# Performance work log

Measured on AMD Instinct MI355X. Metric: run time of the kernel, lower is better.

The kernel has to match this reference:

```python
import jax, jax.numpy as jnp
import numpy as np

EPS = 0.1
MAX_ITER = 100
THRESH = 0.1


def setup_inputs() -> dict:
    key = jax.random.key(0)
    k1, k2, k3, k4 = jax.random.split(key, 4)
    N, P1, P2, D = 4, 1024, 1024, 16
    x = jax.random.normal(k1, (N, P1, D), dtype=jnp.float32)
    y = jax.random.normal(k2, (N, P2, D), dtype=jnp.float32)
    wx = jax.random.uniform(k3, (N, P1), dtype=jnp.float32)
    wy = jax.random.uniform(k4, (N, P2), dtype=jnp.float32)
    # normalize to probability weights (typical usage for empirical measures)
    wx = wx / jnp.sum(wx, axis=-1, keepdims=True)
    wy = wy / jnp.sum(wy, axis=-1, keepdims=True)
    return {"x": x, "y": y, "wx": wx, "wy": wy}


def _cost_matrix(x, y):
    # |x_i - y_j|^1 summed over feature dim -> [N, P1, P2]
    return jnp.sum(jnp.abs(x[:, :, None, :] - y[:, None, :, :]), axis=-1)


def reference(x, y, wx, wy):
    C = _cost_matrix(x, y)                     # [N, P1, P2]
    mu, nu = wx, wy                            # [N, P1], [N, P2]
    log_mu = jnp.log(mu + 1e-8)
    log_nu = jnp.log(nu + 1e-8)

    def M(u, v):
        # (-C_ij + u_i + v_j) / eps
        return (-C + u[:, :, None] + v[:, None, :]) / EPS

    def step(carry, _):
        u, v, done = carry
        u_new = EPS * (log_mu - jax.nn.logsumexp(M(u, v), axis=-1)) + u
        v_new = EPS * (log_nu - jax.nn.logsumexp(M(u_new, v), axis=-2)) + v
        err = jnp.mean(jnp.sum(jnp.abs(u_new - u), axis=-1))
        # emulate torch's early break: freeze u,v once converged
        u_out = jnp.where(done, u, u_new)
        v_out = jnp.where(done, v, v_new)
        done = done | (err < THRESH)
        return (u_out, v_out, done), None

    u0 = jnp.zeros_like(mu)
    v0 = jnp.zeros_like(nu)
    (u, v, _), _ = jax.lax.scan(step, (u0, v0, jnp.array(False)), None, length=MAX_ITER)

    pi = jnp.exp(M(u, v))                      # transport plan [N, P1, P2]
    cost = jnp.sum(pi * C, axis=(-2, -1))      # [N]  (reduction='none')
    return cost, pi, C
```

## Files before the change

### kernel.cpp

```cpp
#include <hip/hip_runtime.h>

static constexpr int   NB      = 4;
static constexpr int   PP      = 1024;
static constexpr int   DD      = 16;
static constexpr float EPSV    = 0.1f;
static constexpr float KE      = 14.42695041f;
static constexpr float KL      = 0.0693147181f;
static constexpr int   MAXIT   = 100;
static constexpr float THRESHV = 0.1f;

static constexpr int NBLK = 256;
static constexpr int NTHR = 512;
static constexpr unsigned DONEG = 1000000u;

__device__ __forceinline__ float fexp2(float v) { return __builtin_amdgcn_exp2f(v); }
__device__ __forceinline__ float flog2(float v) { return __builtin_amdgcn_logf(v); }

static constexpr int    ERR_F_OFF     = 4352;
static constexpr size_t WS_ZERO_BYTES = 4352 * 4;
static constexpr size_t ERR_BYTES    = 512 * 4;

static constexpr int VSNAP_OFF = 131072;

__device__ __forceinline__ float aload(const float* p) {
    return __hip_atomic_load(p, __ATOMIC_RELAXED, __HIP_MEMORY_SCOPE_AGENT);
}
__device__ __forceinline__ void astore(float* p, float v) {
    __hip_atomic_store(p, v, __ATOMIC_RELAXED, __HIP_MEMORY_SCOPE_AGENT);
}
__device__ __forceinline__ unsigned aloadu(const unsigned* p) {
    return __hip_atomic_load(p, __ATOMIC_RELAXED, __HIP_MEMORY_SCOPE_AGENT);
}
__device__ __forceinline__ void astoreu(unsigned* p, unsigned v) {
    __hip_atomic_store(p, v, __ATOMIC_RELAXED, __HIP_MEMORY_SCOPE_AGENT);
}
__device__ __forceinline__ float2 aload2(const float* p) {
    unsigned long long v = __hip_atomic_load((const unsigned long long*)p,
                                             __ATOMIC_RELAXED, __HIP_MEMORY_SCOPE_AGENT);
    union { unsigned long long u; float f[2]; } c; c.u = v;
    return make_float2(c.f[0], c.f[1]);
}
__device__ __forceinline__ void astore2(float* p, float a, float b) {
    union { unsigned long long u; float f[2]; } c; c.f[0] = a; c.f[1] = b;
    __hip_atomic_store((unsigned long long*)p, c.u,
                       __ATOMIC_RELAXED, __HIP_MEMORY_SCOPE_AGENT);
}

__device__ __forceinline__ void gbar_group(unsigned* ws32, int n, int g, unsigned gen) {
    __syncthreads();
    if (threadIdx.x < 64) {
        if (threadIdx.x == 0) astoreu(ws32 + (n * 64 + g) * 16, gen);
        const unsigned* sp = ws32 + (n * 64 + threadIdx.x) * 16;
        while (__ballot(aloadu(sp) >= gen) != ~0ull)
            __builtin_amdgcn_s_sleep(1);
    }
    __syncthreads();
}

__global__ __launch_bounds__(NTHR, 2)
void sinkhorn_kernel(const float* __restrict__ x, const float* __restrict__ y,
                     const float* __restrict__ wx, const float* __restrict__ wy,
                     float* __restrict__ out, float* __restrict__ ws)
{
    __shared__ float rt[16 * PP];
    __shared__ float sbuf[PP];
    __shared__ float cred[8];
    __shared__ int   Ts;

    unsigned* ws32  = (unsigned*)ws;
    unsigned* Tslot = ws32 + 4096;
    unsigned* exitf = ws32 + 4104;
    float*    ews   = ws + ERR_F_OFF;

    float* out_cost = out;
    float* out_pi   = out + NB;
    float* out_C    = out + NB + (size_t)NB * PP * PP;

    const int b   = blockIdx.x;
    const int n   = b >> 6;
    const int g   = b & 63;
    const int i0  = g * 16;
    const int w   = threadIdx.x >> 6;
    const int l   = threadIdx.x & 63;
    const int tid = threadIdx.x;

    float* sc = out_C + (size_t)n * PP * PP;

    float4 xr[2][4];
    #pragma unroll
    for (int rr = 0; rr < 2; ++rr) {
        const float4* xp = (const float4*)(x + ((size_t)n * PP + (i0 + 2 * w + rr)) * DD);
        #pragma unroll
        for (int q = 0; q < 4; ++q) xr[rr][q] = xp[q];
    }
    #pragma unroll 4
    for (int k = 0; k < 16; ++k) {
        int j = l + 64 * k;
        const float4* yp = (const float4*)(y + ((size_t)n * PP + j) * DD);
        float4 y0 = yp[0], y1 = yp[1], y2 = yp[2], y3 = yp[3];
        #pragma unroll
        for (int rr = 0; rr < 2; ++rr) {
            float c = fabsf(xr[rr][0].x - y0.x) + fabsf(xr[rr][0].y - y0.y)
                    + fabsf(xr[rr][0].z - y0.z) + fabsf(xr[rr][0].w - y0.w)
                    + fabsf(xr[rr][1].x - y1.x) + fabsf(xr[rr][1].y - y1.y)
                    + fabsf(xr[rr][1].z - y1.z) + fabsf(xr[rr][1].w - y1.w)
                    + fabsf(xr[rr][2].x - y2.x) + fabsf(xr[rr][2].y - y2.y)
                    + fabsf(xr[rr][2].z - y2.z) + fabsf(xr[rr][2].w - y2.w)
                    + fabsf(xr[rr][3].x - y3.x) + fabsf(xr[rr][3].y - y3.y)
                    + fabsf(xr[rr][3].z - y3.z) + fabsf(xr[rr][3].w - y3.w);
            rt[(2 * w + rr) * PP + j] = c;
        }
    }

    float4 yc[2][4];
    #pragma unroll
    for (int c = 0; c < 2; ++c) {
        const float4* yp = (const float4*)(y + ((size_t)n * PP + (i0 + 2 * w + c)) * DD);
        #pragma unroll
        for (int q = 0; q < 4; ++q) yc[c][q] = yp[q];
    }
    float2 c2[16];
    #pragma unroll 4
    for (int k = 0; k < 16; ++k) {
        const float4* xp = (const float4*)(x + ((size_t)n * PP + (l + 64 * k)) * DD);
        float4 x0 = xp[0], x1 = xp[1], x2 = xp[2], x3 = xp[3];
        float cc[2];
        #pragma unroll
        for (int c = 0; c < 2; ++c) {
            cc[c] = fabsf(x0.x - yc[c][0].x) + fabsf(x0.y - yc[c][0].y)
                  + fabsf(x0.z - yc[c][0].z) + fabsf(x0.w - yc[c][0].w)
                  + fabsf(x1.x - yc[c][1].x) + fabsf(x1.y - yc[c][1].y)
                  + fabsf(x1.z - yc[c][1].z) + fabsf(x1.w - yc[c][1].w)
                  + fabsf(x2.x - yc[c][2].x) + fabsf(x2.y - yc[c][2].y)
                  + fabsf(x2.z - yc[c][2].z) + fabsf(x2.w - yc[c][2].w)
                  + fabsf(x3.x - yc[c][3].x) + fabsf(x3.y - yc[c][3].y)
                  + fabsf(x3.z - yc[c][3].z) + fabsf(x3.w - yc[c][3].w);
        }
        c2[k] = make_float2(cc[0], cc[1]);
    }

    float lmu[2], lnu[2];
    #pragma unroll
    for (int rr = 0; rr < 2; ++rr) {
        lmu[rr] = __logf(wx[n * PP + i0 + 2 * w + rr] + 1e-8f);
        lnu[rr] = __logf(wy[n * PP + i0 + 2 * w + rr] + 1e-8f);
    }

    float uprev0 = 0.f, uprev1 = 0.f;

    #pragma unroll 1
    for (int t = 0; t < MAXIT; ++t) {
        if (t >= 2) {
            unsigned ef = aloadu(exitf + n);
            if (ef != 0u && t >= (int)ef + 1) break;
        }

        if (t == 0) {
            sbuf[2 * tid] = 0.f; sbuf[2 * tid + 1] = 0.f;
        } else {
            float2 vp = aload2(sc + VSNAP_OFF + (size_t)(t - 1) * PP + 2 * tid);
            sbuf[2 * tid] = vp.x; sbuf[2 * tid + 1] = vp.y;
        }
        __syncthreads();

        {
            float4 tt[2][4];
            float m0 = -3.4e38f, m1 = -3.4e38f;
            #pragma unroll
            for (int k = 0; k < 4; ++k) {
                int j = 256 * k + 4 * l;
                float4 v4 = *(const float4*)&sbuf[j];
                float4 ca = *(const float4*)&rt[(2 * w) * PP + j];
                float4 cb = *(const float4*)&rt[(2 * w + 1) * PP + j];
                tt[0][k] = make_float4(v4.x - ca.x, v4.y - ca.y, v4.z - ca.z, v4.w - ca.w);
                tt[1][k] = make_float4(v4.x - cb.x, v4.y - cb.y, v4.z - cb.z, v4.w - cb.w);
                m0 = fmaxf(m0, fmaxf(fmaxf(tt[0][k].x, tt[0][k].y), fmaxf(tt[0][k].z, tt[0][k].w)));
                m1 = fmaxf(m1, fmaxf(fmaxf(tt[1][k].x, tt[1][k].y), fmaxf(tt[1][k].z, tt[1][k].w)));
            }
            #pragma unroll
            for (int off = 32; off >= 1; off >>= 1) {
                m0 = fmaxf(m0, __shfl_xor(m0, off));
                m1 = fmaxf(m1, __shfl_xor(m1, off));
            }
            float s0 = 0.f, s1 = 0.f;
            #pragma unroll
            for (int k = 0; k < 4; ++k) {
                s0 += fexp2((tt[0][k].x - m0) * KE) + fexp2((tt[0][k].y - m0) * KE)
                    + fexp2((tt[0][k].z - m0) * KE) + fexp2((tt[0][k].w - m0) * KE);
                s1 += fexp2((tt[1][k].x - m1) * KE) + fexp2((tt[1][k].y - m1) * KE)
                    + fexp2((tt[1][k].z - m1) * KE) + fexp2((tt[1][k].w - m1) * KE);
            }
            #pragma unroll
            for (int off = 32; off >= 1; off >>= 1) {
                s0 += __shfl_xor(s0, off);
                s1 += __shfl_xor(s1, off);
            }
            float un0 = EPSV * lmu[0] - (m0 + KL * flog2(s0));
            float un1 = EPSV * lmu[1] - (m1 + KL * flog2(s1));
            if (l == 0) astore2(sc + (size_t)t * PP + i0 + 2 * w, un0, un1);
        }

        gbar_group(ws32, n, g, (unsigned)(2 * t + 1));

        {
            float2 up = aload2(sc + (size_t)t * PP + 2 * tid);
            sbuf[2 * tid] = up.x; sbuf[2 * tid + 1] = up.y;
            float we = fabsf(up.x - uprev0) + fabsf(up.y - uprev1);
            uprev0 = up.x; uprev1 = up.y;
            #pragma unroll
            for (int off = 32; off >= 1; off >>= 1) we += __shfl_xor(we, off);
            if (l == 0) cred[w] = we;
        }
        __syncthreads();

        {
            float tt0[16], tt1[16], m0 = -3.4e38f, m1 = -3.4e38f;
            #pragma unroll
            for (int k = 0; k < 16; ++k) {
                float uu = sbuf[l + 64 * k];
                tt0[k] = uu - c2[k].x;
                tt1[k] = uu - c2[k].y;
                m0 = fmaxf(m0, tt0[k]);
                m1 = fmaxf(m1, tt1[k]);
            }
            #pragma unroll
            for (int off = 32; off >= 1; off >>= 1) {
                m0 = fmaxf(m0, __shfl_xor(m0, off));
                m1 = fmaxf(m1, __shfl_xor(m1, off));
            }
            float s0 = 0.f, s1 = 0.f;
            #pragma unroll
            for (int k = 0; k < 16; ++k) {
                s0 += fexp2((tt0[k] - m0) * KE);
                s1 += fexp2((tt1[k] - m1) * KE);
            }
            #pragma unroll
            for (int off = 32; off >= 1; off >>= 1) {
                s0 += __shfl_xor(s0, off);
                s1 += __shfl_xor(s1, off);
            }
            float vn0 = EPSV * lnu[0] - (m0 + KL * flog2(s0));
            float vn1 = EPSV * lnu[1] - (m1 + KL * flog2(s1));
            if (l == 0)
                astore2(sc + VSNAP_OFF + (size_t)t * PP + i0 + 2 * w, vn0, vn1);
        }
        if (g == 0 && tid == 0) {
            float es = cred[0] + cred[1] + cred[2] + cred[3]
                     + cred[4] + cred[5] + cred[6] + cred[7];
            astore(ews + n * 128 + t, es);
        }

        __syncthreads();
        if (tid < 64) {
            if (tid == 0) astoreu(ws32 + (n * 64 + g) * 16, (unsigned)(2 * t + 2));
            if (g == 0) {
                float s1f = aload(ews + 0 * 128 + tid) + aload(ews + 1 * 128 + tid)
                          + aload(ews + 2 * 128 + tid) + aload(ews + 3 * 128 + tid);
                float s2f = aload(ews + 0 * 128 + 64 + tid) + aload(ews + 1 * 128 + 64 + tid)
                          + aload(ews + 2 * 128 + 64 + tid) + aload(ews + 3 * 128 + 64 + tid);
                unsigned long long bb = __ballot(s1f < THRESHV * (float)NB)
                                      | __ballot(s2f < THRESHV * (float)NB);
                if (bb != 0ull && tid == 0 && aloadu(exitf + n) == 0u)
                    astoreu(exitf + n, (unsigned)(t + 1));
            }
            const unsigned* sp = ws32 + (n * 64 + tid) * 16;
            while (__ballot(aloadu(sp) >= (unsigned)(2 * t + 2)) != ~0ull)
                __builtin_amdgcn_s_sleep(1);
        }
        __syncthreads();
    }

    if (g == 0 && tid == 0) astoreu(ws32 + (n * 64) * 16, DONEG);

    if (b == 0 && tid < 64) {
        for (;;) {
            bool ok = (tid >= 4) || (aloadu(ws32 + tid * 64 * 16) >= DONEG);
            if (__ballot(ok) == ~0ull) break;
            __builtin_amdgcn_s_sleep(2);
        }
        float s1f = aload(ews + 0 * 128 + tid) + aload(ews + 1 * 128 + tid)
                  + aload(ews + 2 * 128 + tid) + aload(ews + 3 * 128 + tid);
        float s2f = aload(ews + 0 * 128 + 64 + tid) + aload(ews + 1 * 128 + 64 + tid)
                  + aload(ews + 2 * 128 + 64 + tid) + aload(ews + 3 * 128 + 64 + tid);
        unsigned long long b1 = __ballot(s1f < THRESHV * (float)NB);
        unsigned long long b2 = __ballot(s2f < THRESHV * (float)NB);
        int T = b1 ? (__ffsll((long long)b1) - 1)
                   : (b2 ? 64 + (__ffsll((long long)b2) - 1) : MAXIT - 1);
        if (tid == 0) astoreu(Tslot, (unsigned)(T + 1));
    }
    if (tid == 0) {
        unsigned tv;
        while ((tv = aloadu(Tslot)) == 0u) __builtin_amdgcn_s_sleep(2);
        Ts = (int)tv - 1;
    }
    __syncthreads();
    const int T = Ts;

    float u_loc[2];
    {
        float2 up = aload2(sc + (size_t)T * PP + i0 + 2 * w);
        u_loc[0] = up.x; u_loc[1] = up.y;
        float2 vp = aload2(sc + VSNAP_OFF + (size_t)T * PP + 2 * tid);
        sbuf[2 * tid] = vp.x; sbuf[2 * tid + 1] = vp.y;
    }
    gbar_group(ws32, n, g, DONEG + 1u);

    float cacc = 0.f;
    #pragma unroll
    for (int rr = 0; rr < 2; ++rr) {
        int r = 2 * w + rr;
        int i = i0 + r;
        float un = u_loc[rr];
        #pragma unroll
        for (int k = 0; k < 4; ++k) {
            int j = 256 * k + 4 * l;
            float4 c4 = *(const float4*)&rt[r * PP + j];
            float4 v4 = *(const float4*)&sbuf[j];
            float4 p4;
            p4.x = fexp2((un + v4.x - c4.x) * KE);
            p4.y = fexp2((un + v4.y - c4.y) * KE);
            p4.z = fexp2((un + v4.z - c4.z) * KE);
            p4.w = fexp2((un + v4.w - c4.w) * KE);
            *(float4*)&out_pi[((size_t)n * PP + i) * PP + j] = p4;
            *(float4*)&out_C [((size_t)n * PP + i) * PP + j] = c4;
            cacc += p4.x * c4.x + p4.y * c4.y + p4.z * c4.z + p4.w * c4.w;
        }
    }
    #pragma unroll
    for (int off = 32; off >= 1; off >>= 1) cacc += __shfl_xor(cacc, off);
    if (l == 0) cred[w] = cacc;
    __syncthreads();
    if (tid == 0) {
        float s = 0.f;
        #pragma unroll
        for (int q = 0; q < 8; ++q) s += cred[q];
        atomicAdd(&out_cost[n], s);
    }
}

extern "C" void kernel_launch(void* const* d_in, const int* in_sizes, int n_in,
                              void* d_out, int out_size, void* d_ws, size_t ws_size,
                              hipStream_t stream) {
    const float* x  = (const float*)d_in[0];
    const float* y  = (const float*)d_in[1];
    const float* wx = (const float*)d_in[2];
    const float* wy = (const float*)d_in[3];
    float* out = (float*)d_out;
    float* ws  = (float*)d_ws;

    (void)hipMemsetAsync(d_ws, 0, WS_ZERO_BYTES, stream);
    (void)hipMemsetAsync((char*)d_ws + WS_ZERO_BYTES, 0x7f, ERR_BYTES, stream);
    (void)hipMemsetAsync(d_out, 0, NB * sizeof(float), stream);

    hipLaunchKernelGGL(sinkhorn_kernel, dim3(NBLK), dim3(NTHR), 0, stream,
                       x, y, wx, wy, out, ws);
}
```

Measured before the change: 805.4 us.

## Replace flag-polling group barriers with atomic counters and fold convergence into split barrier

Swaps the per-block generation-flag barrier, which needs a 64-lane ballot poll, for atomic fetch-add counters, one per iteration phase, kept in scratch space inside the C output region. The end-of-iteration barrier becomes split: blocks arrive without waiting and only wait at the start of the next iteration. The convergence flag is packed into the high bits of that counter, so the separate exit-flag word and its global round trip go away. In exchange a large memset over the output region is added at launch to zero the counters, and correctness depends on that scratch area being overwritten later.

```diff
diff --git a/kernel.cpp b/kernel.cpp
--- a/kernel.cpp
+++ b/kernel.cpp
@@ -13,14 +13,16 @@
 static constexpr int NTHR = 512;
 static constexpr unsigned DONEG = 1000000u;
 
+static constexpr int    ERR_F_OFF     = 4352;
+static constexpr size_t WS_ZERO_BYTES = 4352 * 4;
+static constexpr size_t ERR_BYTES     = 512 * 4;
+
+static constexpr int    VSNAP_OFF = 131072;
+static constexpr int    CNT_F_OFF = 786432;
+static constexpr size_t CNT_BYTES = (size_t)2 * MAXIT * 64;
+
 __device__ __forceinline__ float fexp2(float v) { return __builtin_amdgcn_exp2f(v); }
 __device__ __forceinline__ float flog2(float v) { return __builtin_amdgcn_logf(v); }
-
-static constexpr int    ERR_F_OFF     = 4352;
-static constexpr size_t WS_ZERO_BYTES = 4352 * 4;
-static constexpr size_t ERR_BYTES    = 512 * 4;
-
-static constexpr int VSNAP_OFF = 131072;
 
 __device__ __forceinline__ float aload(const float* p) {
     return __hip_atomic_load(p, __ATOMIC_RELAXED, __HIP_MEMORY_SCOPE_AGENT);
@@ -44,6 +46,9 @@
     union { unsigned long long u; float f[2]; } c; c.f[0] = a; c.f[1] = b;
     __hip_atomic_store((unsigned long long*)p, c.u,
                        __ATOMIC_RELAXED, __HIP_MEMORY_SCOPE_AGENT);
+}
+__device__ __forceinline__ void aadd(unsigned* p, unsigned v) {
+    (void)__hip_atomic_fetch_add(p, v, __ATOMIC_RELAXED, __HIP_MEMORY_SCOPE_AGENT);
 }
 
 __device__ __forceinline__ void gbar_group(unsigned* ws32, int n, int g, unsigned gen) {
@@ -66,10 +71,11 @@
     __shared__ float sbuf[PP];
     __shared__ float cred[8];
     __shared__ int   Ts;
+    __shared__ int   s_ex;
+    __shared__ int   s_fired;
 
     unsigned* ws32  = (unsigned*)ws;
     unsigned* Tslot = ws32 + 4096;
-    unsigned* exitf = ws32 + 4104;
     float*    ews   = ws + ERR_F_OFF;
 
     float* out_cost = out;
@@ -85,6 +91,9 @@
     const int tid = threadIdx.x;
 
     float* sc = out_C + (size_t)n * PP * PP;
+    unsigned* cnt = (unsigned*)(sc + CNT_F_OFF);
+
+    if (tid == 0) { s_ex = 0; s_fired = 0; }
 
     float4 xr[2][4];
     #pragma unroll
@@ -150,14 +159,18 @@
 
     #pragma unroll 1
     for (int t = 0; t < MAXIT; ++t) {
-        if (t >= 2) {
-            unsigned ef = aloadu(exitf + n);
-            if (ef != 0u && t >= (int)ef + 1) break;
-        }
-
         if (t == 0) {
             sbuf[2 * tid] = 0.f; sbuf[2 * tid + 1] = 0.f;
         } else {
+            if (tid == 0) {
+                const unsigned* cp = cnt + (unsigned)(2 * (t - 1) + 1) * 16;
+                unsigned cv;
+                while (((cv = aloadu(cp)) & 0xFFFFu) != 64u)
+                    __builtin_amdgcn_s_sleep(1);
+                s_ex = (int)(cv >> 16);
+            }
+            __syncthreads();
+            if (s_ex != 0) break;
             float2 vp = aload2(sc + VSNAP_OFF + (size_t)(t - 1) * PP + 2 * tid);
             sbuf[2 * tid] = vp.x; sbuf[2 * tid + 1] = vp.y;
         }
@@ -199,8 +212,13 @@
             float un1 = EPSV * lmu[1] - (m1 + KL * flog2(s1));
             if (l == 0) astore2(sc + (size_t)t * PP + i0 + 2 * w, un0, un1);
         }
-
-        gbar_group(ws32, n, g, (unsigned)(2 * t + 1));
+        __syncthreads();
+        if (tid == 0) {
+            unsigned* cp = cnt + (unsigned)(2 * t) * 16;
+            aadd(cp, 1u);
+            while ((aloadu(cp) & 0xFFFFu) != 64u) __builtin_amdgcn_s_sleep(1);
+        }
+        __syncthreads();
 
         {
             float2 up = aload2(sc + (size_t)t * PP + 2 * tid);
@@ -249,25 +267,30 @@
                      + cred[4] + cred[5] + cred[6] + cred[7];
             astore(ews + n * 128 + t, es);
         }
-
-        __syncthreads();
-        if (tid < 64) {
-            if (tid == 0) astoreu(ws32 + (n * 64 + g) * 16, (unsigned)(2 * t + 2));
-            if (g == 0) {
-                float s1f = aload(ews + 0 * 128 + tid) + aload(ews + 1 * 128 + tid)
-                          + aload(ews + 2 * 128 + tid) + aload(ews + 3 * 128 + tid);
-                float s2f = aload(ews + 0 * 128 + 64 + tid) + aload(ews + 1 * 128 + 64 + tid)
-                          + aload(ews + 2 * 128 + 64 + tid) + aload(ews + 3 * 128 + 64 + tid);
-                unsigned long long bb = __ballot(s1f < THRESHV * (float)NB)
-                                      | __ballot(s2f < THRESHV * (float)NB);
-                if (bb != 0ull && tid == 0 && aloadu(exitf + n) == 0u)
-                    astoreu(exitf + n, (unsigned)(t + 1));
-            }
-            const unsigned* sp = ws32 + (n * 64 + tid) * 16;
-            while (__ballot(aloadu(sp) >= (unsigned)(2 * t + 2)) != ~0ull)
-                __builtin_amdgcn_s_sleep(1);
-        }
-        __syncthreads();
+        if (g == 0 && s_fired == 0 && tid < 64) {
+            float esl = cred[0] + cred[1] + cred[2] + cred[3]
+                      + cred[4] + cred[5] + cred[6] + cred[7];
+            float s1f = 0.f, s2f = 0.f;
+            #pragma unroll
+            for (int q = 0; q < NB; ++q) {
+                float e1 = aload(ews + q * 128 + tid);
+                float e2 = aload(ews + q * 128 + 64 + tid);
+                if (q == n) {
+                    if (tid == t)      e1 = esl;
+                    if (64 + tid == t) e2 = esl;
+                }
+                s1f += e1; s2f += e2;
+            }
+            unsigned long long bb = __ballot(s1f < THRESHV * (float)NB)
+                                  | __ballot(s2f < THRESHV * (float)NB);
+            if (tid == 0 && bb != 0ull) s_fired = 1;
+        }
+
+        __syncthreads();
+        if (tid == 0) {
+            unsigned addv = 1u + ((g == 0 && s_fired != 0) ? 65536u : 0u);
+            aadd(cnt + (unsigned)(2 * t + 1) * 16, addv);
+        }
     }
 
     if (g == 0 && tid == 0) astoreu(ws32 + (n * 64) * 16, DONEG);
@@ -351,6 +374,12 @@
     (void)hipMemsetAsync(d_ws, 0, WS_ZERO_BYTES, stream);
     (void)hipMemsetAsync((char*)d_ws + WS_ZERO_BYTES, 0x7f, ERR_BYTES, stream);
     (void)hipMemsetAsync(d_out, 0, NB * sizeof(float), stream);
+    {
+        size_t out_C_off = ((size_t)NB + (size_t)NB * PP * PP) * sizeof(float);
+        size_t start = out_C_off + (size_t)CNT_F_OFF * sizeof(float);
+        size_t span  = (size_t)(NB - 1) * PP * PP * sizeof(float) + CNT_BYTES;
+        (void)hipMemsetAsync((char*)d_out + start, 0, span, stream);
+    }
 
     hipLaunchKernelGGL(sinkhorn_kernel, dim3(NBLK), dim3(NTHR), 0, stream,
                        x, y, wx, wy, out, ws);
```

After: 842.2 us. +4.6%, slower.
